# Kernel tuning notes

Measured on AMD Instinct MI355X. Metric: run time of the kernel, lower is better.

The kernel has to match this reference:

```python
import jax, jax.numpy as jnp
import numpy as np

D = 512
B, S1, S2 = 8, 2048, 2048


def setup_inputs() -> dict:
    key = jax.random.key(0)
    ks = jax.random.split(key, 8)
    s = 1.0 / np.sqrt(D)
    return {
        "x1": jax.random.normal(ks[0], (B, S1, D), dtype=jnp.float32),
        "x2": jax.random.normal(ks[1], (B, S2, D), dtype=jnp.float32),
        "Wq": jax.random.normal(ks[2], (D, D), dtype=jnp.float32) * s,
        "bq": jnp.zeros((D,), dtype=jnp.float32),
        "Wk": jax.random.normal(ks[3], (D, D), dtype=jnp.float32) * s,
        "bk": jnp.zeros((D,), dtype=jnp.float32),
        "Wv": jax.random.normal(ks[4], (D, D), dtype=jnp.float32) * s,
        "bv": jnp.zeros((D,), dtype=jnp.float32),
    }


def reference(x1, x2, Wq, bq, Wk, bk, Wv, bv):
    # q,k,v projections (torch Linear: x @ W^T + b)
    q = jnp.einsum("bsd,ed->bse", x1, Wq) + bq  # [B,S1,D]
    k = jnp.einsum("btd,ed->bte", x2, Wk) + bk  # [B,S2,D]
    v = jnp.einsum("btd,ed->bte", x2, Wv) + bv  # [B,S2,D]
    # NOTE: source scales by input_dim (D), not sqrt(D)
    scores = jnp.einsum("bse,bte->bst", q, k) / D  # [B,S1,S2]
    attn = jax.nn.softmax(scores, axis=-1)
    return jnp.einsum("bst,bte->bse", attn, v)  # [B,S1,D]
```

## Files before the change

### kernel.cpp

```cpp
#include <hip/hip_runtime.h>

using u8  = unsigned char;
using u16 = unsigned short;
using u32 = unsigned int;
using s16x8 = __attribute__((ext_vector_type(8))) short;
using bf16x8 = __attribute__((ext_vector_type(8))) __bf16;
using f32x4 = __attribute__((ext_vector_type(4))) float;
using i32x4 = __attribute__((ext_vector_type(4))) int;
using i32x8 = __attribute__((ext_vector_type(8))) int;

__device__ inline u16 f2bf(float f) {
  u32 u = __float_as_uint(f);
  u = (u + 0x7FFFu + ((u >> 16) & 1u)) >> 16;
  return (u16)u;
}

__device__ inline u8 f2fp8(float f) {
  return (u8)(__builtin_amdgcn_cvt_pk_fp8_f32(f, f, 0, false) & 0xFF);
}

__device__ inline f32x4 mfma16(s16x8 a, s16x8 b, f32x4 c) {
  return __builtin_amdgcn_mfma_f32_16x16x32_bf16(
      __builtin_bit_cast(bf16x8, a), __builtin_bit_cast(bf16x8, b), c, 0, 0, 0);
}

__device__ inline f32x4 mfma_fp8(i32x8 a, i32x8 b, f32x4 c) {
  return __builtin_amdgcn_mfma_scale_f32_16x16x128_f8f6f4(
      a, b, c, 0 , 0 , 0, 127, 0, 127);
}

__device__ inline void load_lds16(const void* g, void* l) {
  __builtin_amdgcn_global_load_lds(
      (const __attribute__((address_space(1))) void*)g,
      (__attribute__((address_space(3))) void*)l, 16, 0, 0);
}

__global__ __launch_bounds__(256) void cast_x12(
    const float* __restrict__ x1, const float* __restrict__ x2,
    u16* __restrict__ o1, u16* __restrict__ o2) {
  const float* in = blockIdx.y ? x2 : x1;
  u16* out = blockIdx.y ? o2 : o1;
  int i = (blockIdx.x * 256 + threadIdx.x) * 4;
  float4 f = *(const float4*)(in + i);
  ushort4 o;
  o.x = f2bf(f.x); o.y = f2bf(f.y); o.z = f2bf(f.z); o.w = f2bf(f.w);
  *(ushort4*)(out + i) = o;
}

__global__ __launch_bounds__(256) void cast_w3z(
    const float* __restrict__ a, const float* __restrict__ b,
    const float* __restrict__ c, u16* __restrict__ oa, u16* __restrict__ ob,
    u16* __restrict__ oc) {
  const float* in = blockIdx.y == 0 ? a : (blockIdx.y == 1 ? b : c);
  u16* out = blockIdx.y == 0 ? oa : (blockIdx.y == 1 ? ob : oc);
  int i = (blockIdx.x * 256 + threadIdx.x) * 4;
  float4 f = *(const float4*)(in + i);
  ushort4 o;
  o.x = f2bf(f.x); o.y = f2bf(f.y); o.z = f2bf(f.z); o.w = f2bf(f.w);
  *(ushort4*)(out + i) = o;
}

template <int EPI>
__global__ __launch_bounds__(256) void gemm64(
    const u16* __restrict__ A, const u16* __restrict__ B,
    const u16* __restrict__ B2, void* __restrict__ C, void* __restrict__ C2,
    const float* __restrict__ bias, const float* __restrict__ bias2,
    int M, int N, int K, long sA, long sB, long sC) {
  const int bz = blockIdx.z;
  const int nwg = gridDim.x * gridDim.y;
  int flat = blockIdx.x + gridDim.x * blockIdx.y;
  flat = (flat & 7) * (nwg >> 3) + (flat >> 3);
  const int m0 = (flat / gridDim.x) * 128;
  const int n0 = (flat % gridDim.x) * 128;
  const u16* Ab = A + (size_t)bz * sA;
  const u16* Bsel = (EPI == 4 && n0 >= 512) ? B2 : B;
  const int nb = (EPI == 4 && n0 >= 512) ? n0 - 512 : n0;
  const u16* Bb = Bsel + (size_t)bz * sB;
  const int tid = threadIdx.x;
  const int lane = tid & 63;
  const int wave = tid >> 6;
  const int wm = (wave >> 1) * 64;
  const int wn = (wave & 1) * 64;

  __shared__ u16 SM[128 * 64 * 2];
  u16* As = SM;
  u16* Bs = SM + 128 * 64;

  const int sr = lane >> 3;
  const int gd = (lane & 7) ^ sr;
  const int ch0 = wave * 4;

  f32x4 acc[4][4];
#pragma unroll
  for (int i = 0; i < 4; ++i)
#pragma unroll
    for (int j = 0; j < 4; ++j) acc[i][j] = 0.0f;

  const int fr = lane & 15;
  const int fg = lane >> 4;

  for (int k0 = 0; k0 < K; k0 += 64) {
#pragma unroll
    for (int it = 0; it < 4; ++it) {
      const int ch = ch0 + it;
      const int row = ch * 8 + sr;
      load_lds16(Ab + (size_t)(m0 + row) * K + k0 + gd * 8, &As[ch * 512]);
      load_lds16(Bb + (size_t)(nb + row) * K + k0 + gd * 8, &Bs[ch * 512]);
    }
    __syncthreads();
#pragma unroll
    for (int s = 0; s < 2; ++s) {
      const int slot = ((s * 4 + fg) ^ (fr & 7)) * 8;
      s16x8 af[4], bfr[4];
#pragma unroll
      for (int i = 0; i < 4; ++i) {
        af[i]  = *(const s16x8*)&As[(wm + i * 16 + fr) * 64 + slot];
        bfr[i] = *(const s16x8*)&Bs[(wn + i * 16 + fr) * 64 + slot];
      }
#pragma unroll
      for (int mi = 0; mi < 4; ++mi)
#pragma unroll
        for (int ni = 0; ni < 4; ++ni)
          acc[mi][ni] = mfma16(af[mi], bfr[ni], acc[mi][ni]);
    }
    __syncthreads();
  }

  const int er = fg * 4;
  const int ec = fr;

  if (EPI == 0) {
    u8* Cb = (u8*)C;
#pragma unroll
    for (int mi = 0; mi < 4; ++mi)
#pragma unroll
      for (int ni = 0; ni < 4; ++ni) {
        const int col = n0 + wn + ni * 16 + ec;
        const float badd = bias[col];
#pragma unroll
        for (int i = 0; i < 4; ++i) {
          const int row = m0 + wm + mi * 16 + er + i;
          Cb[(size_t)row * N + col] = f2fp8(acc[mi][ni][i] + badd);
        }
      }
  } else {
    if (n0 < 512) {
      u8* Cb = (u8*)C;
#pragma unroll
      for (int mi = 0; mi < 4; ++mi)
#pragma unroll
        for (int ni = 0; ni < 4; ++ni) {
          const int col = n0 + wn + ni * 16 + ec;
          const float badd = bias[col];
#pragma unroll
          for (int i = 0; i < 4; ++i) {
            const int row = m0 + wm + mi * 16 + er + i;
            Cb[(size_t)row * 512 + col] = f2fp8(acc[mi][ni][i] + badd);
          }
        }
    } else {
      u16* Tb = SM;
      const int batch = m0 >> 11;
      const int srow = m0 & 2047;
      u16* Cv = (u16*)C2 + (size_t)batch * (512 * 2048);
#pragma unroll
      for (int h = 0; h < 2; ++h) {
        if ((wn >> 6) == h) {
#pragma unroll
          for (int mi = 0; mi < 4; ++mi)
#pragma unroll
            for (int ni = 0; ni < 4; ++ni) {
              const int c = ni * 16 + ec;
              const float badd = bias2[n0 - 512 + wn + c];
#pragma unroll
              for (int i = 0; i < 4; ++i) {
                const int r = wm + mi * 16 + er + i;
                Tb[c * 136 + r] = f2bf(acc[mi][ni][i] + badd);
              }
            }
        }
        __syncthreads();
        const int d = tid >> 2;
        const int sc = (tid & 3) * 32;
        const int dglob = n0 - 512 + 64 * h + d;
#pragma unroll
        for (int j = 0; j < 4; ++j) {
          uint4 v = *(const uint4*)&Tb[d * 136 + sc + j * 8];
          *(uint4*)&Cv[(size_t)dglob * 2048 + srow + sc + j * 8] = v;
        }
        __syncthreads();
      }
    }
  }
}

__global__ __launch_bounds__(512, 2) void attn_fused(
    const u8* __restrict__ q8, const u8* __restrict__ k8,
    const u16* __restrict__ vT, float* __restrict__ out) {
  const int batch = blockIdx.x;
  const int q0 = blockIdx.y * 64;
  const u8* qb = q8 + ((size_t)batch * 2048 + q0) * 512;
  const u8* kb = k8 + (size_t)batch * 2048 * 512;
  const u16* vb = vT + (size_t)batch * 512 * 2048;
  float* ob = out + ((size_t)batch * 2048 + q0) * 512;

  const int tid = threadIdx.x;
  const int lane = tid & 63;
  const int wave = tid >> 6;
  const int wm = (wave >> 1) * 16;
  const int wn = (wave & 1) * 32;
  const int wd = wave * 64;
  const int sr = lane >> 3;
  const int gd = (lane & 7) ^ sr;
  const int fr = lane & 15;
  const int fg = lane >> 4;
  const int r7 = fr & 7;
  const int s0 = (2 * fg) ^ r7;
  const int s1 = s0 ^ 1;

  __shared__ u8 Ks[2][4][8192];
  __shared__ u16 Ps[2][64 * 64];

  i32x8 Qf[4];
#pragma unroll
  for (int kc = 0; kc < 4; ++kc) {
    const u8* p = qb + (size_t)(wm + fr) * 512 + kc * 128 + fg * 32;
    i32x4 lo = *(const i32x4*)p;
    i32x4 hi = *(const i32x4*)(p + 16);
    i32x8 q;
    q[0] = lo[0]; q[1] = lo[1]; q[2] = lo[2]; q[3] = lo[3];
    q[4] = hi[0]; q[5] = hi[1]; q[6] = hi[2]; q[7] = hi[3];
    Qf[kc] = q;
  }

  auto stageK = [&](int kv0, int buf) {
#pragma unroll
    for (int it = 0; it < 4; ++it) {
      const int idx = wave * 4 + it;
      const int kc = idx >> 3, sub = idx & 7;
      load_lds16(kb + (size_t)(kv0 + sub * 8 + sr) * 512 + kc * 128 + gd * 16,
                 &Ks[buf][kc][sub * 1024]);
    }
  };
  s16x8 Vr[8];
  auto loadV = [&](int kv0) {
#pragma unroll
    for (int ks = 0; ks < 2; ++ks)
#pragma unroll
      for (int ni = 0; ni < 4; ++ni)
        Vr[ks * 4 + ni] = *(const s16x8*)&vb[(size_t)(wd + ni * 16 + fr) * 2048 +
                                             kv0 + ks * 32 + fg * 8];
  };

  f32x4 oacc[4][4];
#pragma unroll
  for (int i = 0; i < 4; ++i)
#pragma unroll
    for (int j = 0; j < 4; ++j) oacc[i][j] = 0.0f;
  float l_reg[4] = {0.0f, 0.0f, 0.0f, 0.0f};

  constexpr int NT = 32;

  auto tile = [&](int t, int psel) {
    f32x4 sacc[2];
    sacc[0] = 0.0f; sacc[1] = 0.0f;
#pragma unroll
    for (int kc = 0; kc < 4; ++kc) {
#pragma unroll
      for (int ni = 0; ni < 2; ++ni) {
        const u8* pb = &Ks[psel][kc][(wn + ni * 16 + fr) * 128];
        i32x4 blo = *(const i32x4*)(pb + s0 * 16);
        i32x4 bhi = *(const i32x4*)(pb + s1 * 16);
        i32x8 bK;
        bK[0] = blo[0]; bK[1] = blo[1]; bK[2] = blo[2]; bK[3] = blo[3];
        bK[4] = bhi[0]; bK[5] = bhi[1]; bK[6] = bhi[2]; bK[7] = bhi[3];
        sacc[ni] = mfma_fp8(Qf[kc], bK, sacc[ni]);
      }
    }
    u16* Pd = &Ps[psel][0];
#pragma unroll
    for (int ni = 0; ni < 2; ++ni) {
      const int g = (wn >> 3) + ni * 2 + (fr >> 3);
      const int co = fr & 7;
#pragma unroll
      for (int i = 0; i < 4; ++i) {
        const int r = wm + fg * 4 + i;
        const float p = __expf(sacc[ni][i] * (1.0f / 512.0f));
        l_reg[i] += p;
        Pd[r * 64 + ((g ^ (r & 7)) << 3) + co] = f2bf(p);
      }
    }
    __syncthreads();
    if (t + 2 < NT) stageK((t + 2) * 64, psel);
#pragma unroll
    for (int ks = 0; ks < 2; ++ks) {
      s16x8 pa[4];
#pragma unroll
      for (int mi = 0; mi < 4; ++mi) {
        const int r = mi * 16 + fr;
        pa[mi] = *(const s16x8*)&Pd[r * 64 + (((ks * 4 + fg) ^ (r & 7)) << 3)];
      }
#pragma unroll
      for (int ni = 0; ni < 4; ++ni)
#pragma unroll
        for (int mi = 0; mi < 4; ++mi)
          oacc[mi][ni] = mfma16(pa[mi], Vr[ks * 4 + ni], oacc[mi][ni]);
    }
    if (t + 1 < NT) loadV((t + 1) * 64);
  };

  stageK(0, 0);
  loadV(0);
  __syncthreads();
  stageK(64, 1);

  for (int tt = 0; tt < NT; tt += 2) {
    tile(tt, 0);
    tile(tt + 1, 1);
  }

  float* lsc = (float*)&Ps[0][0];
  __syncthreads();
#pragma unroll
  for (int i = 0; i < 4; ++i) {
    float rs = l_reg[i];
    rs += __shfl_xor(rs, 1);
    rs += __shfl_xor(rs, 2);
    rs += __shfl_xor(rs, 4);
    rs += __shfl_xor(rs, 8);
    if (fr == 0) lsc[(wn >> 5) * 64 + wm + fg * 4 + i] = rs;
  }
  __syncthreads();

#pragma unroll
  for (int mi = 0; mi < 4; ++mi)
#pragma unroll
    for (int i = 0; i < 4; ++i) {
      const int r = mi * 16 + fg * 4 + i;
      const float l = lsc[r] + lsc[64 + r];
      const float li = __builtin_amdgcn_rcpf(l);
#pragma unroll
      for (int ni = 0; ni < 4; ++ni)
        ob[(size_t)r * 512 + wd + ni * 16 + fr] = oacc[mi][ni][i] * li;
    }
}

extern "C" void kernel_launch(void* const* d_in, const int* in_sizes, int n_in,
                              void* d_out, int out_size, void* d_ws, size_t ws_size,
                              hipStream_t stream) {
  constexpr int B = 8, S = 2048, D = 512;
  constexpr size_t MS = (size_t)B * S;

  const float* x1 = (const float*)d_in[0];
  const float* x2 = (const float*)d_in[1];
  const float* Wq = (const float*)d_in[2];
  const float* bq = (const float*)d_in[3];
  const float* Wk = (const float*)d_in[4];
  const float* bk = (const float*)d_in[5];
  const float* Wv = (const float*)d_in[6];
  const float* bv = (const float*)d_in[7];
  float* out = (float*)d_out;

  u16* x1b = (u16*)d_ws;
  u16* x2b = x1b + MS * D;
  u16* Wqb = x2b + MS * D;
  u16* Wkb = Wqb + (size_t)D * D;
  u16* Wvb = Wkb + (size_t)D * D;
  u16* vTb = Wvb + (size_t)D * D;
  u16* Sc  = vTb + MS * D;
  float* lbuf = (float*)(Sc + (size_t)B * S * S);
  u8* qb8 = (u8*)(lbuf + MS);
  u8* kb8 = qb8 + MS * D;

  dim3 blk(256);

  cast_x12<<<dim3((MS * D) / 1024, 2), blk, 0, stream>>>(x1, x2, x1b, x2b);
  cast_w3z<<<dim3((D * D) / 1024, 3), blk, 0, stream>>>(
      Wq, Wk, Wv, Wqb, Wkb, Wvb);

  gemm64<0><<<dim3(4, 128, 1), blk, 0, stream>>>(
      x1b, Wqb, nullptr, qb8, nullptr, bq, nullptr,
      16384, 512, 512, 0, 0, 0);

  gemm64<4><<<dim3(8, 128, 1), blk, 0, stream>>>(
      x2b, Wkb, Wvb, kb8, vTb, bk, bv,
      16384, 512, 512, 0, 0, 0);

  attn_fused<<<dim3(8, 32, 1), dim3(512), 0, stream>>>(qb8, kb8, vTb, out);
}
```

Baseline: 265.4 us.

## Fuse fp32-to-bf16 input cast into a single QKV projection GEMM

Removes the separate x1/x2 bf16 cast kernel. A single GEMM launch now loads fp32 activations straight into LDS and converts them to bf16 in registers with packed cvt instructions, covering the Q, K and V projections. This drops a full write and re-read of the bf16 activation copies and one launch, at the cost of twice the LDS traffic for the A operand. The attention kernel also changes the P-tile swizzle pattern to reduce bank conflicts and raises wave priority around its MFMA blocks.

New measurement: 259.6 us. 1.02x faster.

```diff
diff --git a/kernel.cpp b/kernel.cpp
--- a/kernel.cpp
+++ b/kernel.cpp
@@ -35,16 +35,15 @@
       (__attribute__((address_space(3))) void*)l, 16, 0, 0);
 }
 
-__global__ __launch_bounds__(256) void cast_x12(
-    const float* __restrict__ x1, const float* __restrict__ x2,
-    u16* __restrict__ o1, u16* __restrict__ o2) {
-  const float* in = blockIdx.y ? x2 : x1;
-  u16* out = blockIdx.y ? o2 : o1;
-  int i = (blockIdx.x * 256 + threadIdx.x) * 4;
-  float4 f = *(const float4*)(in + i);
-  ushort4 o;
-  o.x = f2bf(f.x); o.y = f2bf(f.y); o.z = f2bf(f.z); o.w = f2bf(f.w);
-  *(ushort4*)(out + i) = o;
+__device__ inline s16x8 cvt8(f32x4 lo, f32x4 hi) {
+  u32 w0, w1, w2, w3;
+  asm("v_cvt_pk_bf16_f32 %0, %1, %2" : "=v"(w0) : "v"(lo[0]), "v"(lo[1]));
+  asm("v_cvt_pk_bf16_f32 %0, %1, %2" : "=v"(w1) : "v"(lo[2]), "v"(lo[3]));
+  asm("v_cvt_pk_bf16_f32 %0, %1, %2" : "=v"(w2) : "v"(hi[0]), "v"(hi[1]));
+  asm("v_cvt_pk_bf16_f32 %0, %1, %2" : "=v"(w3) : "v"(hi[2]), "v"(hi[3]));
+  i32x4 r;
+  r[0] = (int)w0; r[1] = (int)w1; r[2] = (int)w2; r[3] = (int)w3;
+  return __builtin_bit_cast(s16x8, r);
 }
 
 __global__ __launch_bounds__(256) void cast_w3z(
@@ -60,61 +59,69 @@
   *(ushort4*)(out + i) = o;
 }
 
-template <int EPI>
-__global__ __launch_bounds__(256) void gemm64(
-    const u16* __restrict__ A, const u16* __restrict__ B,
-    const u16* __restrict__ B2, void* __restrict__ C, void* __restrict__ C2,
-    const float* __restrict__ bias, const float* __restrict__ bias2,
-    int M, int N, int K, long sA, long sB, long sC) {
-  const int bz = blockIdx.z;
-  const int nwg = gridDim.x * gridDim.y;
-  int flat = blockIdx.x + gridDim.x * blockIdx.y;
-  flat = (flat & 7) * (nwg >> 3) + (flat >> 3);
-  const int m0 = (flat / gridDim.x) * 128;
-  const int n0 = (flat % gridDim.x) * 128;
-  const u16* Ab = A + (size_t)bz * sA;
-  const u16* Bsel = (EPI == 4 && n0 >= 512) ? B2 : B;
-  const int nb = (EPI == 4 && n0 >= 512) ? n0 - 512 : n0;
-  const u16* Bb = Bsel + (size_t)bz * sB;
+__global__ __launch_bounds__(256) void gemm_qkv(
+    const float* __restrict__ x1, const float* __restrict__ x2,
+    const u16* __restrict__ Wq, const u16* __restrict__ Wk,
+    const u16* __restrict__ Wv, u8* __restrict__ qb8, u8* __restrict__ kb8,
+    u16* __restrict__ vTb, const float* __restrict__ bq,
+    const float* __restrict__ bk, const float* __restrict__ bv) {
+  int flat = blockIdx.x + 12 * blockIdx.y;
+  flat = (flat & 7) * 192 + (flat >> 3);
+  const int col = flat % 12;
+  const int m0 = (flat / 12) * 128;
+
+  const float* Ax; const u16* Bw; const float* bias; int n0w, mode;
+  if (col < 4)      { Ax = x1; Bw = Wq; bias = bq; n0w = col * 128;       mode = 0; }
+  else if (col < 8) { Ax = x2; Bw = Wk; bias = bk; n0w = (col - 4) * 128; mode = 1; }
+  else              { Ax = x2; Bw = Wv; bias = bv; n0w = (col - 8) * 128; mode = 2; }
+
   const int tid = threadIdx.x;
   const int lane = tid & 63;
   const int wave = tid >> 6;
   const int wm = (wave >> 1) * 64;
   const int wn = (wave & 1) * 64;
 
-  __shared__ u16 SM[128 * 64 * 2];
-  u16* As = SM;
-  u16* Bs = SM + 128 * 64;
+  __shared__ float Asf[128 * 64];
+  __shared__ u16 Bs[128 * 64];
 
   const int sr = lane >> 3;
   const int gd = (lane & 7) ^ sr;
-  const int ch0 = wave * 4;
-
-  f32x4 acc[4][4];
-#pragma unroll
-  for (int i = 0; i < 4; ++i)
-#pragma unroll
-    for (int j = 0; j < 4; ++j) acc[i][j] = 0.0f;
-
   const int fr = lane & 15;
   const int fg = lane >> 4;
 
-  for (int k0 = 0; k0 < K; k0 += 64) {
+  f32x4 acc[4][4];
+#pragma unroll
+  for (int i = 0; i < 4; ++i)
+#pragma unroll
+    for (int j = 0; j < 4; ++j) acc[i][j] = 0.0f;
+
+  for (int k0 = 0; k0 < 512; k0 += 64) {
+#pragma unroll
+    for (int it = 0; it < 8; ++it) {
+      const int idx = wave * 8 + it;
+      const int row = idx * 4 + (lane >> 4);
+      const int gs = (lane & 15) ^ (row & 15);
+      load_lds16(Ax + (size_t)(m0 + row) * 512 + k0 + gs * 4, &Asf[idx * 256]);
+    }
 #pragma unroll
     for (int it = 0; it < 4; ++it) {
-      const int ch = ch0 + it;
-      const int row = ch * 8 + sr;
-      load_lds16(Ab + (size_t)(m0 + row) * K + k0 + gd * 8, &As[ch * 512]);
-      load_lds16(Bb + (size_t)(nb + row) * K + k0 + gd * 8, &Bs[ch * 512]);
+      const int ch = wave * 4 + it;
+      const int rowb = ch * 8 + sr;
+      load_lds16(Bw + (size_t)(n0w + rowb) * 512 + k0 + gd * 8, &Bs[ch * 512]);
     }
     __syncthreads();
 #pragma unroll
     for (int s = 0; s < 2; ++s) {
-      const int slot = ((s * 4 + fg) ^ (fr & 7)) * 8;
       s16x8 af[4], bfr[4];
 #pragma unroll
       for (int i = 0; i < 4; ++i) {
-        af[i]  = *(const s16x8*)&As[(wm + i * 16 + fr) * 64 + slot];
+        const int rowa = wm + i * 16 + fr;
+        const float* Ar = &Asf[rowa * 64];
+        const int g0 = 2 * (s * 4 + fg);
+        f32x4 lo = *(const f32x4*)&Ar[(g0 ^ fr) * 4];
+        f32x4 hi = *(const f32x4*)&Ar[((g0 + 1) ^ fr) * 4];
+        af[i] = cvt8(lo, hi);
+        const int slot = ((s * 4 + fg) ^ (fr & 7)) * 8;
         bfr[i] = *(const s16x8*)&Bs[(wn + i * 16 + fr) * 64 + slot];
       }
 #pragma unroll
@@ -129,67 +136,51 @@
   const int er = fg * 4;
   const int ec = fr;
 
-  if (EPI == 0) {
-    u8* Cb = (u8*)C;
+  if (mode != 2) {
+    u8* Cb = (mode == 0) ? qb8 : kb8;
 #pragma unroll
     for (int mi = 0; mi < 4; ++mi)
 #pragma unroll
       for (int ni = 0; ni < 4; ++ni) {
-        const int col = n0 + wn + ni * 16 + ec;
-        const float badd = bias[col];
+        const int colg = n0w + wn + ni * 16 + ec;
+        const float badd = bias[colg];
 #pragma unroll
         for (int i = 0; i < 4; ++i) {
           const int row = m0 + wm + mi * 16 + er + i;
-          Cb[(size_t)row * N + col] = f2fp8(acc[mi][ni][i] + badd);
+          Cb[(size_t)row * 512 + colg] = f2fp8(acc[mi][ni][i] + badd);
         }
       }
   } else {
-    if (n0 < 512) {
-      u8* Cb = (u8*)C;
-#pragma unroll
-      for (int mi = 0; mi < 4; ++mi)
-#pragma unroll
-        for (int ni = 0; ni < 4; ++ni) {
-          const int col = n0 + wn + ni * 16 + ec;
-          const float badd = bias[col];
-#pragma unroll
-          for (int i = 0; i < 4; ++i) {
-            const int row = m0 + wm + mi * 16 + er + i;
-            Cb[(size_t)row * 512 + col] = f2fp8(acc[mi][ni][i] + badd);
+    u16* Tb = (u16*)Asf;
+    const int batch = m0 >> 11;
+    const int srow = m0 & 2047;
+    u16* Cv = vTb + (size_t)batch * (512 * 2048);
+#pragma unroll
+    for (int h = 0; h < 2; ++h) {
+      if ((wn >> 6) == h) {
+#pragma unroll
+        for (int mi = 0; mi < 4; ++mi)
+#pragma unroll
+          for (int ni = 0; ni < 4; ++ni) {
+            const int c = ni * 16 + ec;
+            const float badd = bias[n0w + wn + c];
+#pragma unroll
+            for (int i = 0; i < 4; ++i) {
+              const int r = wm + mi * 16 + er + i;
+              Tb[c * 136 + r] = f2bf(acc[mi][ni][i] + badd);
+            }
           }
-        }
-    } else {
-      u16* Tb = SM;
-      const int batch = m0 >> 11;
-      const int srow = m0 & 2047;
-      u16* Cv = (u16*)C2 + (size_t)batch * (512 * 2048);
-#pragma unroll
-      for (int h = 0; h < 2; ++h) {
-        if ((wn >> 6) == h) {
-#pragma unroll
-          for (int mi = 0; mi < 4; ++mi)
-#pragma unroll
-            for (int ni = 0; ni < 4; ++ni) {
-              const int c = ni * 16 + ec;
-              const float badd = bias2[n0 - 512 + wn + c];
-#pragma unroll
-              for (int i = 0; i < 4; ++i) {
-                const int r = wm + mi * 16 + er + i;
-                Tb[c * 136 + r] = f2bf(acc[mi][ni][i] + badd);
-              }
-            }
-        }
-        __syncthreads();
-        const int d = tid >> 2;
-        const int sc = (tid & 3) * 32;
-        const int dglob = n0 - 512 + 64 * h + d;
-#pragma unroll
-        for (int j = 0; j < 4; ++j) {
-          uint4 v = *(const uint4*)&Tb[d * 136 + sc + j * 8];
-          *(uint4*)&Cv[(size_t)dglob * 2048 + srow + sc + j * 8] = v;
-        }
-        __syncthreads();
-      }
+      }
+      __syncthreads();
+      const int d = tid >> 2;
+      const int sc = (tid & 3) * 32;
+      const int dglob = n0w + 64 * h + d;
+#pragma unroll
+      for (int j = 0; j < 4; ++j) {
+        uint4 v = *(const uint4*)&Tb[d * 136 + sc + j * 8];
+        *(uint4*)&Cv[(size_t)dglob * 2048 + srow + sc + j * 8] = v;
+      }
+      __syncthreads();
     }
   }
 }
@@ -274,7 +265,9 @@
         i32x8 bK;
         bK[0] = blo[0]; bK[1] = blo[1]; bK[2] = blo[2]; bK[3] = blo[3];
         bK[4] = bhi[0]; bK[5] = bhi[1]; bK[6] = bhi[2]; bK[7] = bhi[3];
+        __builtin_amdgcn_s_setprio(1);
         sacc[ni] = mfma_fp8(Qf[kc], bK, sacc[ni]);
+        __builtin_amdgcn_s_setprio(0);
       }
     }
     u16* Pd = &Ps[psel][0];
@@ -285,9 +278,11 @@
 #pragma unroll
       for (int i = 0; i < 4; ++i) {
         const int r = wm + fg * 4 + i;
+        const int ph = ((r >> 2) & 1) * 4 + ((r ^ (r >> 3)) & 1) * 2 +
+                       ((r >> 1) & 1);
         const float p = __expf(sacc[ni][i] * (1.0f / 512.0f));
         l_reg[i] += p;
-        Pd[r * 64 + ((g ^ (r & 7)) << 3) + co] = f2bf(p);
+        Pd[r * 64 + ((g ^ ph) << 3) + co] = f2bf(p);
       }
     }
     __syncthreads();
@@ -298,13 +293,17 @@
 #pragma unroll
       for (int mi = 0; mi < 4; ++mi) {
         const int r = mi * 16 + fr;
-        pa[mi] = *(const s16x8*)&Pd[r * 64 + (((ks * 4 + fg) ^ (r & 7)) << 3)];
-      }
+        const int ph = ((r >> 2) & 1) * 4 + ((r ^ (r >> 3)) & 1) * 2 +
+                       ((r >> 1) & 1);
+        pa[mi] = *(const s16x8*)&Pd[r * 64 + (((ks * 4 + fg) ^ ph) << 3)];
+      }
+      __builtin_amdgcn_s_setprio(1);
 #pragma unroll
       for (int ni = 0; ni < 4; ++ni)
 #pragma unroll
         for (int mi = 0; mi < 4; ++mi)
           oacc[mi][ni] = mfma16(pa[mi], Vr[ks * 4 + ni], oacc[mi][ni]);
+      __builtin_amdgcn_s_setprio(0);
     }
     if (t + 1 < NT) loadV((t + 1) * 64);
   };
@@ -374,17 +373,11 @@
 
   dim3 blk(256);
 
-  cast_x12<<<dim3((MS * D) / 1024, 2), blk, 0, stream>>>(x1, x2, x1b, x2b);
   cast_w3z<<<dim3((D * D) / 1024, 3), blk, 0, stream>>>(
       Wq, Wk, Wv, Wqb, Wkb, Wvb);
 
-  gemm64<0><<<dim3(4, 128, 1), blk, 0, stream>>>(
-      x1b, Wqb, nullptr, qb8, nullptr, bq, nullptr,
-      16384, 512, 512, 0, 0, 0);
-
-  gemm64<4><<<dim3(8, 128, 1), blk, 0, stream>>>(
-      x2b, Wkb, Wvb, kb8, vTb, bk, bv,
-      16384, 512, 512, 0, 0, 0);
+  gemm_qkv<<<dim3(12, 128), blk, 0, stream>>>(
+      x1, x2, Wqb, Wkb, Wvb, qb8, kb8, vTb, bq, bk, bv);
 
   attn_fused<<<dim3(8, 32, 1), dim3(512), 0, stream>>>(qb8, kb8, vTb, out);
 }
```
